# Optimization experiments

Measured on AMD Instinct MI355X. Metric: run time of the kernel, lower is better.

The kernel has to match this reference:

```python
import jax, jax.numpy as jnp
import numpy as np
import math

DIM = 2048
NUM_HEADS = 32
HEAD_DIM = DIM // NUM_HEADS  # 64; HEAD_DIM//2 == NUM_HEADS (required by original rope broadcasting)
SEQ_LEN = 2048
BATCH = 2
ROPE_BASE = 10000.0


def apply_rope(inputs, positions):
    # Faithful to original: positions is [L]; sinusoid broadcasts to [1, L, H/2, 1]
    # and then multiplies [B, L, N, H/2] -- the original code relies on N == H/2.
    head_dim = inputs.shape[-1]
    fraction = 2.0 * jnp.arange(head_dim // 2, dtype=inputs.dtype) / head_dim
    timescale = ROPE_BASE ** fraction                      # [H/2]
    sinusoid = positions[:, None] / timescale[None, None, :]  # [1, L, H/2]
    sinusoid = sinusoid[..., None]                         # [1, L, H/2, 1]
    sin = jnp.sin(sinusoid)
    cos = jnp.cos(sinusoid)
    first, second = jnp.split(inputs, 2, axis=-1)          # each [B, L, N, H/2]
    return jnp.concatenate([first * cos - second * sin,
                            second * cos + first * sin], axis=-1)


def setup_inputs() -> dict:
    key = jax.random.key(0)
    ks = jax.random.split(key, 9)
    s = 0.02
    inp = {
        'x': jax.random.normal(ks[0], (BATCH, SEQ_LEN, DIM), dtype=jnp.float32),
        'wq_w': jax.random.normal(ks[1], (DIM, DIM), dtype=jnp.float32) * s,
        'wq_b': jnp.zeros((DIM,), dtype=jnp.float32),
        'wk_w': jax.random.normal(ks[2], (DIM, DIM), dtype=jnp.float32) * s,
        'wk_b': jnp.zeros((DIM,), dtype=jnp.float32),
        'wv_w': jax.random.normal(ks[3], (DIM, DIM), dtype=jnp.float32) * s,
        'wv_b': jnp.zeros((DIM,), dtype=jnp.float32),
        'wo_w': jax.random.normal(ks[4], (DIM, DIM), dtype=jnp.float32) * s,
        'wo_b': jnp.zeros((DIM,), dtype=jnp.float32),
    }
    return inp


def reference(x, wq_w, wq_b, wk_w, wk_b, wv_w, wv_b, wo_w, wo_b):
    B, L, _ = x.shape
    N, H = NUM_HEADS, HEAD_DIM
    q = (x @ wq_w.T + wq_b).reshape(B, L, N, H)
    k = (x @ wk_w.T + wk_b).reshape(B, L, N, H)
    v = (x @ wv_w.T + wv_b).reshape(B, L, N, H)
    positions = jnp.arange(L, dtype=x.dtype)
    q = apply_rope(q, positions)
    k = apply_rope(k, positions)
    # [B, N, L, H]
    q = q.transpose(0, 2, 1, 3)
    k = k.transpose(0, 2, 1, 3)
    v = v.transpose(0, 2, 1, 3)
    scale = math.sqrt(H)
    scores = jnp.einsum('bnqh,bnkh->bnqk', q, k) / scale   # [B, N, L, L]
    causal = jnp.tril(jnp.ones((L, L), dtype=bool))
    scores = jnp.where(causal[None, None], scores, -jnp.inf)
    attn = jax.nn.softmax(scores, axis=-1)
    context = jnp.einsum('bnqk,bnkh->bnqh', attn, v)        # [B, N, L, H]
    context = context.transpose(0, 2, 1, 3).reshape(B, L, DIM)
    return context @ wo_w.T + wo_b
```

## Files before the change

kernel.cpp:

```cpp
#include <hip/hip_runtime.h>
#include <stdint.h>

#define D_MODEL 2048
#define SEQLEN  2048

typedef float f32x4  __attribute__((ext_vector_type(4)));
typedef float f32x16 __attribute__((ext_vector_type(16)));
typedef int   i32x2  __attribute__((ext_vector_type(2)));
typedef int   i32x4  __attribute__((ext_vector_type(4)));
typedef short s16x4  __attribute__((ext_vector_type(4)));
typedef __bf16 bf16x8 __attribute__((ext_vector_type(8)));

__device__ __forceinline__ unsigned short f2bf(float f) {
  union { float f; uint32_t u; } x; x.f = f;
  uint32_t r = (x.u + 0x7FFFu + ((x.u >> 16) & 1u)) >> 16;
  return (unsigned short)r;
}

__device__ __forceinline__ uint32_t cvtpk(float lo, float hi) {
  uint32_t r;
  asm("v_cvt_pk_bf16_f32 %0, %1, %2" : "=v"(r) : "v"(lo), "v"(hi));
  return r;
}

__device__ __forceinline__ bf16x8 as_bf16x8(i32x4 v) {
  union { i32x4 i; bf16x8 b; } u; u.i = v; return u.b;
}

#define MFMA16(acc, a, b) \
  acc = __builtin_amdgcn_mfma_f32_16x16x32_bf16(as_bf16x8(a), as_bf16x8(b), acc, 0, 0, 0)
#define MFMA32(acc, a, b) \
  acc = __builtin_amdgcn_mfma_f32_32x32x16_bf16(as_bf16x8(a), as_bf16x8(b), acc, 0, 0, 0)

__device__ __forceinline__ void gload16(const void* g, void* lds) {
  __builtin_amdgcn_global_load_lds(
      (const __attribute__((address_space(1))) unsigned int*)(uintptr_t)g,
      (__attribute__((address_space(3))) unsigned int*)(uint32_t)(uintptr_t)lds,
      16, 0, 0);
}

__global__ void cvt_all_k(const float* __restrict__ x,
                          const float* __restrict__ w0, const float* __restrict__ w1,
                          const float* __restrict__ w2, const float* __restrict__ w3,
                          unsigned short* __restrict__ xo,
                          unsigned short* __restrict__ o0, unsigned short* __restrict__ o1,
                          unsigned short* __restrict__ o2, unsigned short* __restrict__ o3) {
  const int i = blockIdx.x * 256 + threadIdx.x;
  const float* src; unsigned short* dst; int off;
  if (i < 2097152) { src = x; dst = xo; off = i; }
  else {
    const int j = i - 2097152, seg = j >> 20;
    off = j & 1048575;
    src = seg == 0 ? w0 : seg == 1 ? w1 : seg == 2 ? w2 : w3;
    dst = seg == 0 ? o0 : seg == 1 ? o1 : seg == 2 ? o2 : o3;
  }
  f32x4 v = *(const f32x4*)&src[(size_t)off * 4];
  s16x4 o;
#pragma unroll
  for (int j = 0; j < 4; ++j) o[j] = (short)f2bf(v[j]);
  *(s16x4*)&dst[(size_t)off * 4] = o;
}

template <bool ROPE, bool F32OUT>
__global__ __launch_bounds__(512) void gemm1(
    const unsigned short* __restrict__ A,
    const unsigned short* __restrict__ W,
    const float* __restrict__ bias,
    unsigned short* __restrict__ Ob,
    float* __restrict__ Of) {
  constexpr int PLANE_E = 384 * 32;
  __shared__ alignas(16) unsigned short L[4 * PLANE_E];

  const int t = threadIdx.x;
  const int w = t >> 6, l = t & 63;
  const int wm = w >> 1, wn = w & 1;
  const int band = l >> 4, ln = l & 15;

  const int m0 = blockIdx.y * 256;
  const int nloc = blockIdx.x * 128;

  auto stage1 = [&](int p, int ktile, int b, int i) {
    unsigned short* dst = L + (b * 2 + p) * PLANE_E;
    const int idx = w * 3 + i;
    const int row = idx * 16 + (l >> 2);
    const int gblk = (l & 3) ^ ((row >> 1) & 3);
    const int kcol = ktile * 64 + p * 32;
    const unsigned short* src =
        (idx < 16) ? &A[(size_t)(m0 + row) * D_MODEL + kcol + gblk * 8]
                   : &W[(size_t)(nloc + row - 256) * D_MODEL + kcol + gblk * 8];
    gload16(src, dst + idx * 512);
  };
  auto ld = [&](const unsigned short* pl, int r) {
    return *(const i32x4*)&pl[r * 32 + (((band ^ (r >> 1)) & 3) << 3)];
  };

  f32x4 acc[4][4] = {};

#pragma unroll
  for (int i = 0; i < 3; ++i) stage1(0, 0, 0, i);
#pragma unroll
  for (int i = 0; i < 3; ++i) stage1(1, 0, 0, i);
  asm volatile("s_waitcnt vmcnt(3)" ::: "memory");
  __builtin_amdgcn_s_barrier();

  for (int kt = 0; kt < 32; ++kt) {
    const int rb = kt & 1;
    const int ktn = (kt + 1) & 31;
#pragma unroll
    for (int kh = 0; kh < 2; ++kh) {
      const unsigned short* pl = L + (rb * 2 + kh) * PLANE_E;
      i32x4 bv[4], av[2];
#pragma unroll
      for (int nf = 0; nf < 4; ++nf) bv[nf] = ld(pl, 256 + wn * 64 + nf * 16 + ln);
#pragma unroll
      for (int mf = 0; mf < 2; ++mf) av[mf] = ld(pl, wm * 64 + mf * 16 + ln);
      stage1(kh, ktn, rb ^ 1, 0);
      stage1(kh, ktn, rb ^ 1, 1);
      __builtin_amdgcn_s_barrier();
      asm volatile("s_waitcnt lgkmcnt(0)" ::: "memory");
      __builtin_amdgcn_sched_barrier(0);
      __builtin_amdgcn_s_setprio(1);
#pragma unroll
      for (int mf = 0; mf < 2; ++mf)
#pragma unroll
        for (int nf = 0; nf < 4; ++nf) MFMA16(acc[mf][nf], av[mf], bv[nf]);
      __builtin_amdgcn_s_setprio(0);
      __builtin_amdgcn_s_barrier();
#pragma unroll
      for (int mf = 0; mf < 2; ++mf) av[mf] = ld(pl, wm * 64 + (2 + mf) * 16 + ln);
      stage1(kh, ktn, rb ^ 1, 2);
      __builtin_amdgcn_s_barrier();
      asm volatile("s_waitcnt lgkmcnt(0)" ::: "memory");
      __builtin_amdgcn_sched_barrier(0);
      __builtin_amdgcn_s_setprio(1);
#pragma unroll
      for (int mf = 0; mf < 2; ++mf)
#pragma unroll
        for (int nf = 0; nf < 4; ++nf) MFMA16(acc[2 + mf][nf], av[mf], bv[nf]);
      __builtin_amdgcn_s_setprio(0);
      asm volatile("s_waitcnt vmcnt(3)" ::: "memory");
      __builtin_amdgcn_s_barrier();
    }
  }
  asm volatile("s_waitcnt vmcnt(0)" ::: "memory");

  float bb[4];
#pragma unroll
  for (int nf = 0; nf < 4; ++nf) bb[nf] = bias[nloc + wn * 64 + nf * 16 + ln];

  const int head = (nloc + wn * 64) >> 6;
  const float ts = powf(10000.0f, (float)head * (1.0f / 32.0f));
#pragma unroll
  for (int am = 0; am < 4; ++am) {
#pragma unroll
    for (int r = 0; r < 4; ++r) {
      const int row = m0 + wm * 64 + am * 16 + band * 4 + r;
      float vals[4];
#pragma unroll
      for (int nf = 0; nf < 4; ++nf) vals[nf] = acc[am][nf][r] + bb[nf];
      if constexpr (ROPE) {
        const float pos = (float)(row & (SEQLEN - 1));
        float sv, cv;
        __sincosf(pos / ts, &sv, &cv);
#pragma unroll
        for (int pp = 0; pp < 2; ++pp) {
          const float f0 = vals[pp], s0 = vals[pp + 2];
          vals[pp]     = f0 * cv - s0 * sv;
          vals[pp + 2] = s0 * cv + f0 * sv;
        }
      }
#pragma unroll
      for (int nf = 0; nf < 4; ++nf) {
        const size_t oi = (size_t)row * D_MODEL + nloc + wn * 64 + nf * 16 + ln;
        if constexpr (F32OUT) Of[oi] = vals[nf];
        else                  Ob[oi] = f2bf(vals[nf]);
      }
    }
  }
}

__global__ __launch_bounds__(256) void attn_fwd(
    const unsigned short* __restrict__ Q, const unsigned short* __restrict__ K,
    const unsigned short* __restrict__ V, unsigned short* __restrict__ O) {
  __shared__ alignas(16) unsigned short Ks[2][64 * 64];
  __shared__ alignas(16) unsigned short Vt[2][64 * 64];

  const int t = threadIdx.x;
  const int w = t >> 6, l = t & 63;
  const int l31 = l & 31, t5 = l >> 5;
  const int bx = blockIdx.x, head = blockIdx.y, b = blockIdx.z;
  const int h0 = head * 64;
  const size_t rb = (size_t)b * SEQLEN;

  const int kdr = l >> 3, kdb = l & 7;

  int vkv[2], vcol[2];
#pragma unroll
  for (int i = 0; i < 2; ++i) {
    const int s = i * 256 + t;
    const int blk = s >> 6;
    const int tau = (s >> 3) & 7;
    vkv[i] = (blk >> 1) * 16 + ((tau >> 1) & 1) * 8 + (tau >> 2) * 4 + ((s & 7) >> 1);
    vcol[i] = (blk & 1) * 32 + (tau & 1) * 16 + (s & 1) * 8;
  }

  auto stageKV = [&](int bb2, int kbase) {
#pragma unroll
    for (int i = 0; i < 2; ++i) {
      const int drow = (i * 4 + w) * 8 + kdr;
      const int sblk = kdb ^ (drow & 7);
      gload16(&K[(rb + kbase + drow) * D_MODEL + h0 + sblk * 8],
              &Ks[bb2][(i * 4 + w) * 512]);
    }
#pragma unroll
    for (int i = 0; i < 2; ++i)
      gload16(&V[(rb + kbase + vkv[i]) * D_MODEL + h0 + vcol[i]],
              &Vt[bb2][i * 2048 + w * 512]);
  };

  for (int pi = 0; pi < 2; ++pi) {
    const int qt = pi ? (15 - bx) : bx;
    const int q0 = qt * 128;
    const int qg = q0 + w * 32 + l31;

    i32x4 qf[4];
#pragma unroll
    for (int hk = 0; hk < 4; ++hk)
      qf[hk] = *(const i32x4*)&Q[(rb + qg) * D_MODEL + h0 + hk * 16 + t5 * 8];

    f32x16 oacc[2] = {};
    float lsum = 0.f;
    const int nkt = qt * 2 + 2;

    stageKV(0, 0);
    asm volatile("s_waitcnt vmcnt(0)" ::: "memory");
    __syncthreads();

    for (int kt = 0; kt < nkt; ++kt) {
      const int cur = kt & 1, nxt = cur ^ 1;
      const int k0 = kt * 64;
      const bool more = (kt + 1 < nkt);

      if (more) stageKV(nxt, k0 + 64);

      f32x16 sacc[2] = {};
#pragma unroll
      for (int kvf = 0; kvf < 2; ++kvf) {
        const int krow = kvf * 32 + l31;
#pragma unroll
        for (int hk = 0; hk < 4; ++hk) {
          i32x4 a = *(const i32x4*)&Ks[cur][krow * 64 + ((2 * hk + t5) ^ (krow & 7)) * 8];
          MFMA32(sacc[kvf], a, qf[hk]);
        }
      }

      i32x2 trr[4][2][2];
      {
        const uint32_t vb0 = (uint32_t)(uintptr_t)&Vt[cur][0] + (uint32_t)(l * 8);
#pragma unroll
        for (int ks = 0; ks < 4; ++ks)
#pragma unroll
          for (int hf = 0; hf < 2; ++hf) {
            const uint32_t ba = vb0 + (ks * 2 + hf) * 1024;
            asm volatile("ds_read_b64_tr_b16 %0, %1"
                         : "=v"(trr[ks][hf][0]) : "v"(ba) : "memory");
            asm volatile("ds_read_b64_tr_b16 %0, %1"
                         : "=v"(trr[ks][hf][1]) : "v"(ba + 512) : "memory");
          }
      }

      const bool needmask = (k0 + 64 > q0 + w * 32);
      uint32_t W[2][4][2];
#pragma unroll
      for (int kvf = 0; kvf < 2; ++kvf)
#pragma unroll
        for (int g = 0; g < 4; ++g)
#pragma unroll
          for (int p = 0; p < 2; ++p) {
            float pv[2];
#pragma unroll
            for (int e = 0; e < 2; ++e) {
              const int reg = 4 * g + 2 * p + e;
              const int kvl = kvf * 32 + 8 * g + 4 * t5 + 2 * p + e;
              pv[e] = exp2f(sacc[kvf][reg] * 0.18033688f);
              if (needmask && (k0 + kvl > qg)) pv[e] = 0.f;
              lsum += pv[e];
            }
            W[kvf][g][p] = cvtpk(pv[0], pv[1]);
          }

#pragma unroll
      for (int ks = 0; ks < 4; ++ks) {
        const int kvf = ks >> 1;
        const int gA = 2 * (ks & 1), gB = gA + 1;
        uint32_t a0 = W[kvf][gA][0], b0 = W[kvf][gB][0];
        uint32_t a1 = W[kvf][gA][1], b1 = W[kvf][gB][1];
        asm("v_permlane32_swap_b32 %0, %1" : "+v"(a0), "+v"(b0));
        asm("v_permlane32_swap_b32 %0, %1" : "+v"(a1), "+v"(b1));
        i32x4 pf;
        pf[0] = (int)a0; pf[1] = (int)a1; pf[2] = (int)b0; pf[3] = (int)b1;
        if (ks == 0)      asm volatile("s_waitcnt lgkmcnt(12)" ::: "memory");
        else if (ks == 1) asm volatile("s_waitcnt lgkmcnt(8)"  ::: "memory");
        else if (ks == 2) asm volatile("s_waitcnt lgkmcnt(4)"  ::: "memory");
        else              asm volatile("s_waitcnt lgkmcnt(0)"  ::: "memory");
        __builtin_amdgcn_sched_barrier(0);
#pragma unroll
        for (int hf = 0; hf < 2; ++hf) {
          i32x4 vbf;
          vbf[0] = trr[ks][hf][0][0]; vbf[1] = trr[ks][hf][0][1];
          vbf[2] = trr[ks][hf][1][0]; vbf[3] = trr[ks][hf][1][1];
          MFMA32(oacc[hf], pf, vbf);
        }
      }

      if (more) asm volatile("s_waitcnt vmcnt(0)" ::: "memory");
      __syncthreads();
    }

    lsum += __shfl_xor(lsum, 32);
    const float inv = 1.0f / lsum;

#pragma unroll
    for (int g2 = 0; g2 < 4; ++g2)
#pragma unroll
      for (int rr = 0; rr < 4; ++rr) {
        const int rowl = rr + 8 * g2 + 4 * t5;
        const float invr = __shfl(inv, (l & 32) + rowl);
        const size_t gr = rb + q0 + w * 32 + rowl;
#pragma unroll
        for (int hf = 0; hf < 2; ++hf)
          O[gr * D_MODEL + h0 + hf * 32 + l31] = f2bf(oacc[hf][4 * g2 + rr] * invr);
      }
  }
}

extern "C" void kernel_launch(void* const* d_in, const int* in_sizes, int n_in,
                              void* d_out, int out_size, void* d_ws, size_t ws_size,
                              hipStream_t stream) {
  const float* x    = (const float*)d_in[0];
  const float* wq_w = (const float*)d_in[1];
  const float* wq_b = (const float*)d_in[2];
  const float* wk_w = (const float*)d_in[3];
  const float* wk_b = (const float*)d_in[4];
  const float* wv_w = (const float*)d_in[5];
  const float* wv_b = (const float*)d_in[6];
  const float* wo_w = (const float*)d_in[7];
  const float* wo_b = (const float*)d_in[8];
  float* out = (float*)d_out;

  unsigned short* ws  = (unsigned short*)d_ws;
  unsigned short* xb  = ws;
  unsigned short* wqb = xb  + 8388608;
  unsigned short* wkb = wqb + 4194304;
  unsigned short* wvb = wkb + 4194304;
  unsigned short* wob = wvb + 4194304;
  unsigned short* qb  = wob + 4194304;
  unsigned short* kb  = qb  + 8388608;
  unsigned short* vb  = kb  + 8388608;
  unsigned short* cb  = xb;

  cvt_all_k<<<24576, 256, 0, stream>>>(x, wq_w, wk_w, wv_w, wo_w,
                                       xb, wqb, wkb, wvb, wob);

  dim3 g(16, 16);
  gemm1<true,  false><<<g, 512, 0, stream>>>(xb, wqb, wq_b, qb, nullptr);
  gemm1<true,  false><<<g, 512, 0, stream>>>(xb, wkb, wk_b, kb, nullptr);
  gemm1<false, false><<<g, 512, 0, stream>>>(xb, wvb, wv_b, vb, nullptr);

  attn_fwd<<<dim3(8, 32, 2), 256, 0, stream>>>(qb, kb, vb, cb);

  gemm1<false, true><<<g, 512, 0, stream>>>(cb, wob, wo_b, nullptr, out);
}
```

Measured before the change: 272.5 us.

## Pre-transpose V in a separate kernel and remap GEMM block order

Adds a kernel that writes V into a per-head transposed [B,N,H,L] buffer, reusing the wq workspace. The attention kernel then stages V tiles with the same swizzled layout as K and reads them with plain ds_read_b128, replacing the ds_read_b64_tr_b16 transposed LDS loads and their staged waitcnts. Separately, the GEMM remaps block indices so consecutive blocks share N columns across M tiles, aiming for better L2 reuse. The trade is an extra launch and an extra pass over V through global memory.

```diff
diff --git a/kernel.cpp b/kernel.cpp
--- a/kernel.cpp
+++ b/kernel.cpp
@@ -6,7 +6,6 @@
 
 typedef float f32x4  __attribute__((ext_vector_type(4)));
 typedef float f32x16 __attribute__((ext_vector_type(16)));
-typedef int   i32x2  __attribute__((ext_vector_type(2)));
 typedef int   i32x4  __attribute__((ext_vector_type(4)));
 typedef short s16x4  __attribute__((ext_vector_type(4)));
 typedef __bf16 bf16x8 __attribute__((ext_vector_type(8)));
@@ -61,6 +60,31 @@
   *(s16x4*)&dst[(size_t)off * 4] = o;
 }
 
+__global__ __launch_bounds__(256) void vtrans_k(
+    const unsigned short* __restrict__ V, unsigned short* __restrict__ VT) {
+  __shared__ alignas(16) unsigned short Lt[64][72];
+  const int t = threadIdx.x;
+  const int s0 = blockIdx.x * 64, head = blockIdx.y, b = blockIdx.z;
+  const size_t vbase = ((size_t)b * SEQLEN + s0) * D_MODEL + head * 64;
+#pragma unroll
+  for (int i = 0; i < 2; ++i) {
+    const int lin = i * 256 + t;
+    const int row = lin >> 3, slot = lin & 7;
+    i32x4 v = *(const i32x4*)&V[vbase + (size_t)row * D_MODEL + slot * 8];
+    union { i32x4 v; unsigned short s[8]; } u; u.v = v;
+#pragma unroll
+    for (int j = 0; j < 8; ++j) Lt[slot * 8 + j][row] = u.s[j];
+  }
+  __syncthreads();
+  const size_t obase = (((size_t)b * 32 + head) * 64) * SEQLEN + s0;
+#pragma unroll
+  for (int i = 0; i < 2; ++i) {
+    const int lin = i * 256 + t;
+    const int d = lin >> 3, sb = lin & 7;
+    *(i32x4*)&VT[obase + (size_t)d * SEQLEN + sb * 8] = *(const i32x4*)&Lt[d][sb * 8];
+  }
+}
+
 template <bool ROPE, bool F32OUT>
 __global__ __launch_bounds__(512) void gemm1(
     const unsigned short* __restrict__ A,
@@ -76,8 +100,9 @@
   const int wm = w >> 1, wn = w & 1;
   const int band = l >> 4, ln = l & 15;
 
-  const int m0 = blockIdx.y * 256;
-  const int nloc = blockIdx.x * 128;
+  const int fid = blockIdx.y * 16 + blockIdx.x;
+  const int m0 = ((fid & 7) + 8 * ((fid >> 3) & 1)) * 256;
+  const int nloc = (fid >> 4) * 128;
 
   auto stage1 = [&](int p, int ktile, int b, int i) {
     unsigned short* dst = L + (b * 2 + p) * PLANE_E;
@@ -181,9 +206,9 @@
 
 __global__ __launch_bounds__(256) void attn_fwd(
     const unsigned short* __restrict__ Q, const unsigned short* __restrict__ K,
-    const unsigned short* __restrict__ V, unsigned short* __restrict__ O) {
+    const unsigned short* __restrict__ VT, unsigned short* __restrict__ O) {
   __shared__ alignas(16) unsigned short Ks[2][64 * 64];
-  __shared__ alignas(16) unsigned short Vt[2][64 * 64];
+  __shared__ alignas(16) unsigned short Vs[2][64 * 64];
 
   const int t = threadIdx.x;
   const int w = t >> 6, l = t & 63;
@@ -191,18 +216,9 @@
   const int bx = blockIdx.x, head = blockIdx.y, b = blockIdx.z;
   const int h0 = head * 64;
   const size_t rb = (size_t)b * SEQLEN;
+  const size_t vtb = ((size_t)b * 32 + head) * 64 * SEQLEN;
 
   const int kdr = l >> 3, kdb = l & 7;
-
-  int vkv[2], vcol[2];
-#pragma unroll
-  for (int i = 0; i < 2; ++i) {
-    const int s = i * 256 + t;
-    const int blk = s >> 6;
-    const int tau = (s >> 3) & 7;
-    vkv[i] = (blk >> 1) * 16 + ((tau >> 1) & 1) * 8 + (tau >> 2) * 4 + ((s & 7) >> 1);
-    vcol[i] = (blk & 1) * 32 + (tau & 1) * 16 + (s & 1) * 8;
-  }
 
   auto stageKV = [&](int bb2, int kbase) {
 #pragma unroll
@@ -213,9 +229,12 @@
               &Ks[bb2][(i * 4 + w) * 512]);
     }
 #pragma unroll
-    for (int i = 0; i < 2; ++i)
-      gload16(&V[(rb + kbase + vkv[i]) * D_MODEL + h0 + vcol[i]],
-              &Vt[bb2][i * 2048 + w * 512]);
+    for (int i = 0; i < 2; ++i) {
+      const int drow = (i * 4 + w) * 8 + kdr;
+      const int sblk = kdb ^ (drow & 7);
+      gload16(&VT[vtb + (size_t)drow * SEQLEN + kbase + sblk * 8],
+              &Vs[bb2][(i * 4 + w) * 512]);
+    }
   };
 
   for (int pi = 0; pi < 2; ++pi) {
@@ -252,21 +271,6 @@
           i32x4 a = *(const i32x4*)&Ks[cur][krow * 64 + ((2 * hk + t5) ^ (krow & 7)) * 8];
           MFMA32(sacc[kvf], a, qf[hk]);
         }
-      }
-
-      i32x2 trr[4][2][2];
-      {
-        const uint32_t vb0 = (uint32_t)(uintptr_t)&Vt[cur][0] + (uint32_t)(l * 8);
-#pragma unroll
-        for (int ks = 0; ks < 4; ++ks)
-#pragma unroll
-          for (int hf = 0; hf < 2; ++hf) {
-            const uint32_t ba = vb0 + (ks * 2 + hf) * 1024;
-            asm volatile("ds_read_b64_tr_b16 %0, %1"
-                         : "=v"(trr[ks][hf][0]) : "v"(ba) : "memory");
-            asm volatile("ds_read_b64_tr_b16 %0, %1"
-                         : "=v"(trr[ks][hf][1]) : "v"(ba + 512) : "memory");
-          }
       }
 
       const bool needmask = (k0 + 64 > q0 + w * 32);
@@ -299,17 +303,12 @@
         asm("v_permlane32_swap_b32 %0, %1" : "+v"(a1), "+v"(b1));
         i32x4 pf;
         pf[0] = (int)a0; pf[1] = (int)a1; pf[2] = (int)b0; pf[3] = (int)b1;
-        if (ks == 0)      asm volatile("s_waitcnt lgkmcnt(12)" ::: "memory");
-        else if (ks == 1) asm volatile("s_waitcnt lgkmcnt(8)"  ::: "memory");
-        else if (ks == 2) asm volatile("s_waitcnt lgkmcnt(4)"  ::: "memory");
-        else              asm volatile("s_waitcnt lgkmcnt(0)"  ::: "memory");
-        __builtin_amdgcn_sched_barrier(0);
 #pragma unroll
         for (int hf = 0; hf < 2; ++hf) {
-          i32x4 vbf;
-          vbf[0] = trr[ks][hf][0][0]; vbf[1] = trr[ks][hf][0][1];
-          vbf[2] = trr[ks][hf][1][0]; vbf[3] = trr[ks][hf][1][1];
-          MFMA32(oacc[hf], pf, vbf);
+          const int vrow = hf * 32 + l31;
+          i32x4 vb = *(const i32x4*)&Vs[cur][vrow * 64 +
+                                             (((2 * ks + t5) ^ (vrow & 7)) << 3)];
+          MFMA32(oacc[hf], pf, vb);
         }
       }
 
@@ -358,6 +357,7 @@
   unsigned short* kb  = qb  + 8388608;
   unsigned short* vb  = kb  + 8388608;
   unsigned short* cb  = xb;
+  unsigned short* vt  = wqb;
 
   cvt_all_k<<<24576, 256, 0, stream>>>(x, wq_w, wk_w, wv_w, wo_w,
                                        xb, wqb, wkb, wvb, wob);
@@ -367,7 +367,9 @@
   gemm1<true,  false><<<g, 512, 0, stream>>>(xb, wkb, wk_b, kb, nullptr);
   gemm1<false, false><<<g, 512, 0, stream>>>(xb, wvb, wv_b, vb, nullptr);
 
-  attn_fwd<<<dim3(8, 32, 2), 256, 0, stream>>>(qb, kb, vb, cb);
+  vtrans_k<<<dim3(32, 32, 2), 256, 0, stream>>>(vb, vt);
+
+  attn_fwd<<<dim3(8, 32, 2), 256, 0, stream>>>(qb, kb, vt, cb);
 
   gemm1<false, true><<<g, 512, 0, stream>>>(cb, wob, wo_b, nullptr, out);
 }
```

Measured after the change: 276.4 us. About the same (+1.4%).
